# Optimization experiments

Hardware: AMD Instinct MI355X
Metric: run time of the kernel (lower is better)

The kernel has to match this reference:

```python
import jax, jax.numpy as jnp
import numpy as np

B, S, H, E, K, DFF = 4, 2048, 1024, 8, 2, 4096


def setup_inputs() -> dict:
    key = jax.random.key(0)
    k0, k1, k2, k3 = jax.random.split(key, 4)
    sc = 0.02
    return {
        "x": jax.random.normal(k0, (B, S, H), jnp.float32),
        "gate_W": jax.random.normal(k1, (H, E), jnp.float32) * sc,
        "gate_b": jnp.zeros((E,), jnp.float32),
        "W1": jax.random.normal(k2, (H, DFF), jnp.float32) * sc,
        "b1": jnp.zeros((DFF,), jnp.float32),
        "W2": jax.random.normal(k3, (DFF, H), jnp.float32) * sc,
        "b2": jnp.zeros((H,), jnp.float32),
    }


def reference(x, gate_W, gate_b, W1, b1, W2, b2):
    b, s, h = x.shape
    x_flat = x.reshape(-1, h)                      # [T, H]
    gate_scores = x_flat @ gate_W + gate_b         # [T, E]
    top_k_scores, top_k_idx = jax.lax.top_k(gate_scores, K)   # [T, K]
    top_k_w = jax.nn.softmax(top_k_scores, axis=-1)           # [T, K]

    # All experts share the same weights (ModuleList reuses one module), so
    # sum_i w_i * expert_i(x) == expert(x) * sum_i w_i. top_k indices are
    # unique per token, so the per-token combine weight is sum of top-k weights.
    hdd = jax.nn.gelu(x_flat @ W1 + b1, approximate=False)    # [T, DFF]
    y = hdd @ W2 + b2                                         # [T, H]
    tok_w = top_k_w.sum(axis=-1)                              # [T] (== 1.0)
    output = (y * tok_w[:, None]).reshape(b, s, h)

    expert_load = gate_scores.mean(axis=0)                    # [E]
    aux_loss = (expert_load ** 2).sum()
    exp_counts = jnp.zeros((E,), jnp.int32).at[top_k_idx.ravel()].add(1)
    return output, aux_loss, exp_counts
```

## Files before the change

### kernel.cpp

```cpp
#include <hip/hip_runtime.h>
#include <hip/hip_bf16.h>
#include <math.h>

#define Tn   8192
#define Hn   1024
#define En   8
#define DFFn 4096

typedef __attribute__((ext_vector_type(8))) short bf16x8;
typedef __attribute__((ext_vector_type(4))) float f32x4;

static __device__ inline unsigned short f2bf(float f) {
    __hip_bfloat16 h = __float2bfloat16(f);
    return __builtin_bit_cast(unsigned short, h);
}

__global__ __launch_bounds__(256) void prep(
    const float* __restrict__ W1, unsigned short* __restrict__ W1t,
    const float* __restrict__ W2, unsigned short* __restrict__ W2t,
    const float* __restrict__ x, const float* __restrict__ gW,
    const float* __restrict__ gb, unsigned short* __restrict__ xbf,
    float* __restrict__ tokw, float* __restrict__ load_sum,
    int* __restrict__ counts)
{
    __shared__ float smem[8 * 1024 + En];
    __shared__ int   s_cnt[En];
    const int tid = threadIdx.x;
    const int id  = blockIdx.x;

    if (id >= 5120) {
        const int tb = id - 5120;
        float* tile = smem;
        const int bx = tb & 31, by = tb >> 5;
        const int n0 = bx * 32, k0 = by * 32;
        const int r  = tid >> 3, c4 = (tid & 7) * 4;
        float4 v = *(const float4*)(W2 + (size_t)(k0 + r) * Hn + n0 + c4);
        tile[(c4 + 0) * 33 + r] = v.x;
        tile[(c4 + 1) * 33 + r] = v.y;
        tile[(c4 + 2) * 33 + r] = v.z;
        tile[(c4 + 3) * 33 + r] = v.w;
        __syncthreads();
        ushort4 pk;
        pk.x = f2bf(tile[r * 33 + c4 + 0]);
        pk.y = f2bf(tile[r * 33 + c4 + 1]);
        pk.z = f2bf(tile[r * 33 + c4 + 2]);
        pk.w = f2bf(tile[r * 33 + c4 + 3]);
        *(ushort4*)(W2t + (size_t)(n0 + r) * DFFn + k0 + c4) = pk;
        return;
    }

    if (id >= 1024) {
        const int tb = id - 1024;
        float* tile = smem;
        const int bx = tb & 127, by = tb >> 7;
        const int n0 = bx * 32, k0 = by * 32;
        const int r  = tid >> 3, c4 = (tid & 7) * 4;
        float4 v = *(const float4*)(W1 + (size_t)(k0 + r) * DFFn + n0 + c4);
        tile[(c4 + 0) * 33 + r] = v.x;
        tile[(c4 + 1) * 33 + r] = v.y;
        tile[(c4 + 2) * 33 + r] = v.z;
        tile[(c4 + 3) * 33 + r] = v.w;
        __syncthreads();
        ushort4 pk;
        pk.x = f2bf(tile[r * 33 + c4 + 0]);
        pk.y = f2bf(tile[r * 33 + c4 + 1]);
        pk.z = f2bf(tile[r * 33 + c4 + 2]);
        pk.w = f2bf(tile[r * 33 + c4 + 3]);
        *(ushort4*)(W1t + (size_t)(n0 + r) * Hn + k0 + c4) = pk;
        return;
    }

    float* gwt    = smem;
    float* s_load = smem + 8 * 1024;
    if (tid < En) { s_load[tid] = 0.f; s_cnt[tid] = 0; }
    #pragma unroll
    for (int i = 0; i < 32; ++i) {
        int f = tid + i * 256;
        gwt[(f & 7) * 1024 + (f >> 3)] = gW[f];
    }
    __syncthreads();

    const int lane = tid & 63;
    const int wv   = tid >> 6;

    for (int tok = id * 4 + wv; tok < Tn; tok += 4096) {
        const float4* xr = (const float4*)(x + (size_t)tok * Hn);
        float acc[8] = {0.f,0.f,0.f,0.f,0.f,0.f,0.f,0.f};
        #pragma unroll
        for (int j = 0; j < Hn / 256; ++j) {
            int h4 = j * 64 + lane;
            float4 xv = xr[h4];
            ushort4 pk;
            pk.x = f2bf(xv.x); pk.y = f2bf(xv.y);
            pk.z = f2bf(xv.z); pk.w = f2bf(xv.w);
            ((ushort4*)xbf)[(size_t)tok * (Hn / 4) + h4] = pk;
            #pragma unroll
            for (int e = 0; e < 8; ++e) {
                const float4 w = *(const float4*)(gwt + e * 1024 + h4 * 4);
                acc[e] += xv.x * w.x + xv.y * w.y + xv.z * w.z + xv.w * w.w;
            }
        }
        #pragma unroll
        for (int e = 0; e < 8; ++e) {
            float v = acc[e];
            #pragma unroll
            for (int off = 32; off > 0; off >>= 1) v += __shfl_xor(v, off, 64);
            acc[e] = v + gb[e];
        }
        if (lane == 0) {
            #pragma unroll
            for (int e = 0; e < 8; ++e) atomicAdd(&s_load[e], acc[e]);
            int i1 = 0; float v1 = acc[0];
            #pragma unroll
            for (int e = 1; e < 8; ++e) if (acc[e] > v1) { v1 = acc[e]; i1 = e; }
            int i2 = -1; float v2 = -3.0e38f;
            #pragma unroll
            for (int e = 0; e < 8; ++e) if (e != i1 && acc[e] > v2) { v2 = acc[e]; i2 = e; }
            atomicAdd(&s_cnt[i1], 1);
            atomicAdd(&s_cnt[i2], 1);
            float e2 = __expf(v2 - v1);
            float t  = 1.0f + e2;
            tokw[tok] = 1.0f / t + e2 / t;
        }
    }
    __syncthreads();
    if (tid < En) {
        atomicAdd(&load_sum[tid], s_load[tid]);
        atomicAdd(&counts[tid],   s_cnt[tid]);
    }
}


static __device__ inline bf16x8 ldsfrag(const char* base, int row, int chunk) {
    return *(const bf16x8*)(base + row * 128 + (((chunk) ^ (row & 7)) << 4));
}

template<int BN, int WM, int WN, int EPI>
__global__ __launch_bounds__(512, 2) void gemm8(
    const __hip_bfloat16* __restrict__ A,
    const __hip_bfloat16* __restrict__ Bt,
    const float* __restrict__ bias,
    const float* __restrict__ tokw,
    void* __restrict__ C, int N, int K, int nx,
    const float* __restrict__ load_sum, const int* __restrict__ counts,
    float* __restrict__ out_tail, int nblk)
{
    constexpr int BM = 256;
    constexpr int MR = (BM / WM) / 16;
    constexpr int NR = (BN / WN) / 16;
    constexpr int AU = BM / 64;
    constexpr int BU = BN / 64;
    constexpr int ABYTES = BM * 64 * 2;
    constexpr int BBYTES = BN * 64 * 2;
    constexpr int TILEB  = ABYTES + BBYTES;

    extern __shared__ char lds[];

    const int tid = threadIdx.x;
    const int id  = blockIdx.x;

    if (EPI == 0 && id >= nblk) {
        if (tid == 0) {
            float aux = 0.f;
            #pragma unroll
            for (int e = 0; e < En; ++e) {
                float m = load_sum[e] * (1.0f / (float)Tn);
                aux += m * m;
            }
            out_tail[0] = aux;
            #pragma unroll
            for (int e = 0; e < En; ++e) out_tail[1 + e] = (float)counts[e];
        }
        return;
    }

    int wg = id;
    { int xcd = wg & 7, idx = wg >> 3; wg = xcd * (nblk >> 3) + idx; }
    const int by = wg / nx, bx = wg % nx;
    const int m0 = by * BM, n0 = bx * BN;

    const int lane = tid & 63;
    const int wid  = tid >> 6;
    const int wn   = wid % WN;
    const int wm   = wid / WN;
    const int wrow = wm * (BM / WM);
    const int wcol = wn * (BN / WN);
    const int fr   = lane & 15;
    const int fq   = lane >> 4;

    const int sr = tid >> 3;
    const int sc = (tid & 7) ^ (sr & 7);
    unsigned aOff[AU], bOff[BU];
    #pragma unroll
    for (int u = 0; u < AU; ++u)
        aOff[u] = (unsigned)((m0 + u * 64 + sr) * K + sc * 8);
    #pragma unroll
    for (int u = 0; u < BU; ++u)
        bOff[u] = (unsigned)((n0 + u * 64 + sr) * K + sc * 8);

#define STA(b, u, kt) __builtin_amdgcn_global_load_lds( \
    (const __attribute__((address_space(1))) void*)(A + aOff[u] + (unsigned)(kt) * 64u), \
    (__attribute__((address_space(3))) void*)(lds + (b) * TILEB + (u) * 8192 + tid * 16), 16, 0, 0)
#define STB(b, u, kt) __builtin_amdgcn_global_load_lds( \
    (const __attribute__((address_space(1))) void*)(Bt + bOff[u] + (unsigned)(kt) * 64u), \
    (__attribute__((address_space(3))) void*)(lds + (b) * TILEB + ABYTES + (u) * 8192 + tid * 16), 16, 0, 0)

    bf16x8 af[MR / 2][2];
    bf16x8 bfr[4][2];
    f32x4  acc[MR][NR];
    const f32x4 zero = {0.f, 0.f, 0.f, 0.f};
    #pragma unroll
    for (int i = 0; i < MR; ++i)
        #pragma unroll
        for (int j = 0; j < NR; ++j) acc[i][j] = zero;

#define RDA(b, half) do { _Pragma("unroll") \
    for (int m_ = 0; m_ < MR / 2; ++m_) { _Pragma("unroll") \
        for (int ks_ = 0; ks_ < 2; ++ks_) \
            af[m_][ks_] = ldsfrag(lds + (b) * TILEB, \
                wrow + ((half) * (MR / 2) + m_) * 16 + fr, ks_ * 4 + fq); } } while (0)

#define RDB(b, half) do { _Pragma("unroll") \
    for (int n_ = 0; n_ < 2; ++n_) { _Pragma("unroll") \
        for (int ks_ = 0; ks_ < 2; ++ks_) \
            bfr[(half) * 2 + n_][ks_] = ldsfrag(lds + (b) * TILEB + ABYTES, \
                wcol + ((half) * 2 + n_) * 16 + fr, ks_ * 4 + fq); } } while (0)

#define MFMAQ(hm, hn) do { \
    __builtin_amdgcn_s_setprio(1); \
    _Pragma("unroll") \
    for (int m_ = 0; m_ < MR / 2; ++m_) { _Pragma("unroll") \
        for (int n_ = 0; n_ < 2; ++n_) { _Pragma("unroll") \
            for (int ks_ = 0; ks_ < 2; ++ks_) \
                acc[(hm) * (MR / 2) + m_][(hn) * 2 + n_] = \
                    __builtin_amdgcn_mfma_f32_16x16x32_bf16( \
                        bfr[(hn) * 2 + n_][ks_], af[m_][ks_], \
                        acc[(hm) * (MR / 2) + m_][(hn) * 2 + n_], 0, 0, 0); } } \
    __builtin_amdgcn_s_setprio(0); } while (0)

#define MFMAQ1(hm) do { \
    __builtin_amdgcn_s_setprio(1); \
    _Pragma("unroll") \
    for (int m_ = 0; m_ < MR / 2; ++m_) { _Pragma("unroll") \
        for (int n_ = 0; n_ < NR; ++n_) { _Pragma("unroll") \
            for (int ks_ = 0; ks_ < 2; ++ks_) \
                acc[(hm) * (MR / 2) + m_][n_] = \
                    __builtin_amdgcn_mfma_f32_16x16x32_bf16( \
                        bfr[n_][ks_], af[m_][ks_], \
                        acc[(hm) * (MR / 2) + m_][n_], 0, 0, 0); } } \
    __builtin_amdgcn_s_setprio(0); } while (0)

#define MIDSYNC do { \
    __builtin_amdgcn_sched_barrier(0); \
    __builtin_amdgcn_s_barrier(); \
    asm volatile("s_waitcnt lgkmcnt(0)" ::: "memory"); \
    __builtin_amdgcn_sched_barrier(0); } while (0)

#define ENDBAR do { \
    __builtin_amdgcn_sched_barrier(0); \
    __builtin_amdgcn_s_barrier(); \
    __builtin_amdgcn_sched_barrier(0); } while (0)

#define DRAIN6 do { asm volatile("s_waitcnt vmcnt(6)" ::: "memory"); \
    __builtin_amdgcn_sched_barrier(0); } while (0)
#define DRAIN2 do { asm volatile("s_waitcnt vmcnt(2)" ::: "memory"); \
    __builtin_amdgcn_sched_barrier(0); } while (0)

    const int KT = K >> 6;

    if constexpr (WM == 2) {
        STA(0,0,0); STA(0,1,0); STA(0,2,0); STA(0,3,0);
        STB(0,0,0); STB(0,1,0); STB(0,2,0); STB(0,3,0);
        STA(1,0,1); STA(1,2,1);
        STB(1,0,1); STB(1,1,1); STB(1,2,1); STB(1,3,1);
        DRAIN6;
        __builtin_amdgcn_s_barrier();
        __builtin_amdgcn_sched_barrier(0);

        for (int i = 0; i < (KT >> 1); ++i) {
            const int t1 = 2 * i + 1;
            const int c2 = (2 * i + 2 < KT) ? 2 * i + 2 : KT - 1;
            const int c3 = (2 * i + 3 < KT) ? 2 * i + 3 : KT - 1;

            RDA(0, 0); RDB(0, 0);
            STA(1,1,t1); STA(1,3,t1);
            MIDSYNC; MFMAQ(0, 0); ENDBAR;
            RDB(0, 1);
            STA(0,0,c2); STA(0,2,c2);
            MIDSYNC; MFMAQ(0, 1); ENDBAR;
            RDA(0, 1);
            STB(0,0,c2); STB(0,1,c2);
            MIDSYNC; MFMAQ(1, 0); ENDBAR;
            STB(0,2,c2); STB(0,3,c2);
            MIDSYNC; MFMAQ(1, 1); DRAIN6; ENDBAR;
            RDA(1, 0); RDB(1, 0);
            STA(0,1,c2); STA(0,3,c2);
            MIDSYNC; MFMAQ(0, 0); ENDBAR;
            RDB(1, 1);
            STA(1,0,c3); STA(1,2,c3);
            MIDSYNC; MFMAQ(0, 1); ENDBAR;
            RDA(1, 1);
            STB(1,0,c3); STB(1,1,c3);
            MIDSYNC; MFMAQ(1, 0); ENDBAR;
            STB(1,2,c3); STB(1,3,c3);
            MIDSYNC; MFMAQ(1, 1); DRAIN6; ENDBAR;
        }
    } else {
        STA(0,0,0); STA(0,1,0); STA(0,2,0); STA(0,3,0);
        STB(0,0,0); STB(0,1,0);
        STB(1,0,1); STB(1,1,1);
        DRAIN2;
        __builtin_amdgcn_s_barrier();
        __builtin_amdgcn_sched_barrier(0);

        for (int i = 0; i < (KT >> 1); ++i) {
            const int t1 = 2 * i + 1;
            const int c2 = (2 * i + 2 < KT) ? 2 * i + 2 : KT - 1;
            const int c3 = (2 * i + 3 < KT) ? 2 * i + 3 : KT - 1;

            RDA(0, 0); RDB(0, 0); RDB(0, 1);
            STA(1,0,t1); STA(1,1,t1); STA(1,2,t1); STA(1,3,t1);
            MIDSYNC; MFMAQ1(0); ENDBAR;
            RDA(0, 1);
            STB(0,0,c2); STB(0,1,c2);
            MIDSYNC; MFMAQ1(1); DRAIN2; ENDBAR;
            RDA(1, 0); RDB(1, 0); RDB(1, 1);
            STA(0,0,c2); STA(0,1,c2); STA(0,2,c2); STA(0,3,c2);
            MIDSYNC; MFMAQ1(0); ENDBAR;
            RDA(1, 1);
            STB(1,0,c3); STB(1,1,c3);
            MIDSYNC; MFMAQ1(1); DRAIN2; ENDBAR;
        }
    }

    const int mrow0 = m0 + wrow + (lane & 15);
    const int ncol0 = n0 + wcol + (lane >> 4) * 4;
    float4 b4[NR];
    #pragma unroll
    for (int ni = 0; ni < NR; ++ni)
        b4[ni] = *(const float4*)(bias + ncol0 + ni * 16);

    #pragma unroll
    for (int mi = 0; mi < MR; ++mi) {
        const int row = mrow0 + mi * 16;
        float tw = 1.0f;
        if constexpr (EPI == 1) tw = tokw[row];
        #pragma unroll
        for (int ni = 0; ni < NR; ++ni) {
            const int cb = ncol0 + ni * 16;
            f32x4 v = acc[mi][ni];
            v[0] += b4[ni].x; v[1] += b4[ni].y;
            v[2] += b4[ni].z; v[3] += b4[ni].w;
            if constexpr (EPI == 0) {
                ushort4 pk;
                #pragma unroll
                for (int j = 0; j < 4; ++j) {
                    float u  = v[j];
                    float uu = u * u;
                    float z  = u * __fmaf_rn(uu, -0.07135607f, -1.59576912f);
                    float e  = __expf(z);
                    float g  = u * __builtin_amdgcn_rcpf(1.0f + e);
                    ((unsigned short*)&pk)[j] = f2bf(g);
                }
                *(ushort4*)((__hip_bfloat16*)C + (size_t)row * N + cb) = pk;
            } else {
                float4 o;
                o.x = v[0] * tw; o.y = v[1] * tw;
                o.z = v[2] * tw; o.w = v[3] * tw;
                *(float4*)((float*)C + (size_t)row * N + cb) = o;
            }
        }
    }

#undef STA
#undef STB
#undef RDA
#undef RDB
#undef MFMAQ
#undef MFMAQ1
#undef MIDSYNC
#undef ENDBAR
#undef DRAIN6
#undef DRAIN2
}

extern "C" void kernel_launch(void* const* d_in, const int* in_sizes, int n_in,
                              void* d_out, int out_size, void* d_ws, size_t ws_size,
                              hipStream_t stream)
{
    const float* x  = (const float*)d_in[0];
    const float* gW = (const float*)d_in[1];
    const float* gb = (const float*)d_in[2];
    const float* W1 = (const float*)d_in[3];
    const float* b1 = (const float*)d_in[4];
    const float* W2 = (const float*)d_in[5];
    const float* b2 = (const float*)d_in[6];
    float* out = (float*)d_out;

    char* ws = (char*)d_ws;
    __hip_bfloat16* xbf = (__hip_bfloat16*)ws;  ws += (size_t)Tn * Hn * 2;
    __hip_bfloat16* W1t = (__hip_bfloat16*)ws;  ws += (size_t)Hn * DFFn * 2;
    __hip_bfloat16* W2t = (__hip_bfloat16*)ws;  ws += (size_t)Hn * DFFn * 2;
    __hip_bfloat16* hdd = (__hip_bfloat16*)ws;  ws += (size_t)Tn * DFFn * 2;
    float* tokw     = (float*)ws;               ws += (size_t)Tn * 4;
    float* load_sum = (float*)ws;               ws += En * 4;
    int*   counts   = (int*)ws;                 ws += En * 4;

    static bool attr_done = false;
    if (!attr_done) {
        (void)hipFuncSetAttribute(
            reinterpret_cast<const void*>(&gemm8<256, 2, 4, 0>),
            hipFuncAttributeMaxDynamicSharedMemorySize, 131072);
        (void)hipFuncSetAttribute(
            reinterpret_cast<const void*>(&gemm8<128, 4, 2, 1>),
            hipFuncAttributeMaxDynamicSharedMemorySize, 98304);
        attr_done = true;
    }

    hipMemsetAsync(load_sum, 0, En * 4 * 2, stream);

    prep<<<9216, 256, 0, stream>>>(W1, (unsigned short*)W1t,
                                   W2, (unsigned short*)W2t,
                                   x, gW, gb, (unsigned short*)xbf,
                                   tokw, load_sum, counts);

    gemm8<256, 2, 4, 0><<<513, 512, 131072, stream>>>(
        xbf, W1t, b1, nullptr, hdd, DFFn, Hn, 16,
        load_sum, counts, out + (size_t)Tn * Hn, 512);

    gemm8<128, 4, 2, 1><<<256, 512, 98304, stream>>>(
        hdd, W2t, b2, tokw, out, Hn, DFFn, 8,
        nullptr, nullptr, nullptr, 256);
}
```

Baseline: 277.2 us.

## Persist first GEMM over two tiles with overlapped epilogue; larger transpose tiles

The weight-transpose part of prep now uses 128x128 tiles with bf16 conversion before an XOR-swizzled LDS transpose and 16-byte stores. This cuts the block count and LDS traffic. The first GEMM launches half as many blocks, and each block processes two output tiles, issuing the next tile's prologue loads before running the GELU epilogue of the current one. The MFMA operand order is swapped so each lane holds a column layout, and the epilogue uses scalar bf16 stores. These scalar stores may be less efficient, and the hand-tuned vmcnt waits carry a correctness risk.

```diff
diff --git a/kernel.cpp b/kernel.cpp
--- a/kernel.cpp
+++ b/kernel.cpp
@@ -8,6 +8,7 @@
 #define DFFn 4096
 
 typedef __attribute__((ext_vector_type(8))) short bf16x8;
+typedef __attribute__((ext_vector_type(8))) unsigned short u16x8;
 typedef __attribute__((ext_vector_type(4))) float f32x4;
 
 static __device__ inline unsigned short f2bf(float f) {
@@ -28,48 +29,42 @@
     const int tid = threadIdx.x;
     const int id  = blockIdx.x;
 
-    if (id >= 5120) {
-        const int tb = id - 5120;
-        float* tile = smem;
-        const int bx = tb & 31, by = tb >> 5;
-        const int n0 = bx * 32, k0 = by * 32;
-        const int r  = tid >> 3, c4 = (tid & 7) * 4;
-        float4 v = *(const float4*)(W2 + (size_t)(k0 + r) * Hn + n0 + c4);
-        tile[(c4 + 0) * 33 + r] = v.x;
-        tile[(c4 + 1) * 33 + r] = v.y;
-        tile[(c4 + 2) * 33 + r] = v.z;
-        tile[(c4 + 3) * 33 + r] = v.w;
+    if (id < 512) {
+        const float* src; unsigned short* dst; int SR, SC, tb;
+        if (id < 256) { src = W1; dst = W1t; SR = Hn;   SC = DFFn; tb = id; }
+        else          { src = W2; dst = W2t; SR = DFFn; SC = Hn;   tb = id - 256; }
+        const int tcs = SC >> 7;
+        const int tr  = tb / tcs, tc = tb - tr * tcs;
+        const int r0  = tr << 7, c0 = tc << 7;
+        unsigned short* tile = (unsigned short*)smem;
+
+        #pragma unroll
+        for (int i = 0; i < 16; ++i) {
+            int idx = tid + i * 256;
+            int r = idx >> 5, c4 = (idx & 31) << 2;
+            float4 v = *(const float4*)(src + (size_t)(r0 + r) * SC + c0 + c4);
+            int cs = c4 ^ (((r >> 3) & 7) << 2);
+            ushort4 pk;
+            pk.x = f2bf(v.x); pk.y = f2bf(v.y);
+            pk.z = f2bf(v.z); pk.w = f2bf(v.w);
+            *(ushort4*)(tile + r * 128 + cs) = pk;
+        }
         __syncthreads();
-        ushort4 pk;
-        pk.x = f2bf(tile[r * 33 + c4 + 0]);
-        pk.y = f2bf(tile[r * 33 + c4 + 1]);
-        pk.z = f2bf(tile[r * 33 + c4 + 2]);
-        pk.w = f2bf(tile[r * 33 + c4 + 3]);
-        *(ushort4*)(W2t + (size_t)(n0 + r) * DFFn + k0 + c4) = pk;
+        #pragma unroll
+        for (int i = 0; i < 8; ++i) {
+            int idx = tid + i * 256;
+            int n = idx >> 4, kg = idx & 15, k0 = kg << 3;
+            int s = (kg & 7) << 2;
+            u16x8 o;
+            #pragma unroll
+            for (int j = 0; j < 8; ++j)
+                o[j] = tile[(k0 + j) * 128 + (n ^ s)];
+            *(u16x8*)(dst + (size_t)(c0 + n) * SR + r0 + k0) = o;
+        }
         return;
     }
 
-    if (id >= 1024) {
-        const int tb = id - 1024;
-        float* tile = smem;
-        const int bx = tb & 127, by = tb >> 7;
-        const int n0 = bx * 32, k0 = by * 32;
-        const int r  = tid >> 3, c4 = (tid & 7) * 4;
-        float4 v = *(const float4*)(W1 + (size_t)(k0 + r) * DFFn + n0 + c4);
-        tile[(c4 + 0) * 33 + r] = v.x;
-        tile[(c4 + 1) * 33 + r] = v.y;
-        tile[(c4 + 2) * 33 + r] = v.z;
-        tile[(c4 + 3) * 33 + r] = v.w;
-        __syncthreads();
-        ushort4 pk;
-        pk.x = f2bf(tile[r * 33 + c4 + 0]);
-        pk.y = f2bf(tile[r * 33 + c4 + 1]);
-        pk.z = f2bf(tile[r * 33 + c4 + 2]);
-        pk.w = f2bf(tile[r * 33 + c4 + 3]);
-        *(ushort4*)(W1t + (size_t)(n0 + r) * Hn + k0 + c4) = pk;
-        return;
-    }
-
+    const int gid = id - 512;
     float* gwt    = smem;
     float* s_load = smem + 8 * 1024;
     if (tid < En) { s_load[tid] = 0.f; s_cnt[tid] = 0; }
@@ -83,7 +78,7 @@
     const int lane = tid & 63;
     const int wv   = tid >> 6;
 
-    for (int tok = id * 4 + wv; tok < Tn; tok += 4096) {
+    for (int tok = gid * 4 + wv; tok < Tn; tok += 4096) {
         const float4* xr = (const float4*)(x + (size_t)tok * Hn);
         float acc[8] = {0.f,0.f,0.f,0.f,0.f,0.f,0.f,0.f};
         #pragma unroll
@@ -130,12 +125,11 @@
     }
 }
 
-
 static __device__ inline bf16x8 ldsfrag(const char* base, int row, int chunk) {
     return *(const bf16x8*)(base + row * 128 + (((chunk) ^ (row & 7)) << 4));
 }
 
-template<int BN, int WM, int WN, int EPI>
+template<int BN, int WM, int WN, int EPI, int TPB>
 __global__ __launch_bounds__(512, 2) void gemm8(
     const __hip_bfloat16* __restrict__ A,
     const __hip_bfloat16* __restrict__ Bt,
@@ -174,11 +168,6 @@
         return;
     }
 
-    int wg = id;
-    { int xcd = wg & 7, idx = wg >> 3; wg = xcd * (nblk >> 3) + idx; }
-    const int by = wg / nx, bx = wg % nx;
-    const int m0 = by * BM, n0 = bx * BN;
-
     const int lane = tid & 63;
     const int wid  = tid >> 6;
     const int wn   = wid % WN;
@@ -190,13 +179,23 @@
 
     const int sr = tid >> 3;
     const int sc = (tid & 7) ^ (sr & 7);
+
+    int m0, n0;
     unsigned aOff[AU], bOff[BU];
-    #pragma unroll
-    for (int u = 0; u < AU; ++u)
-        aOff[u] = (unsigned)((m0 + u * 64 + sr) * K + sc * 8);
-    #pragma unroll
-    for (int u = 0; u < BU; ++u)
-        bOff[u] = (unsigned)((n0 + u * 64 + sr) * K + sc * 8);
+    auto setup = [&](int t) {
+        int g   = id + t * nblk;
+        int xcd = g & 7;
+        int wg  = xcd * ((nblk * TPB) >> 3) + (g >> 3);
+        int by  = wg / nx, bx = wg - by * nx;
+        m0 = by * BM; n0 = bx * BN;
+        #pragma unroll
+        for (int u = 0; u < AU; ++u)
+            aOff[u] = (unsigned)((m0 + u * 64 + sr) * K + sc * 8);
+        #pragma unroll
+        for (int u = 0; u < BU; ++u)
+            bOff[u] = (unsigned)((n0 + u * 64 + sr) * K + sc * 8);
+    };
+    setup(0);
 
 #define STA(b, u, kt) __builtin_amdgcn_global_load_lds( \
     (const __attribute__((address_space(1))) void*)(A + aOff[u] + (unsigned)(kt) * 64u), \
@@ -204,6 +203,12 @@
 #define STB(b, u, kt) __builtin_amdgcn_global_load_lds( \
     (const __attribute__((address_space(1))) void*)(Bt + bOff[u] + (unsigned)(kt) * 64u), \
     (__attribute__((address_space(3))) void*)(lds + (b) * TILEB + ABYTES + (u) * 8192 + tid * 16), 16, 0, 0)
+
+#define PROLOG_G0 do { \
+    STA(0,0,0); STA(0,1,0); STA(0,2,0); STA(0,3,0); \
+    STB(0,0,0); STB(0,1,0); STB(0,2,0); STB(0,3,0); \
+    STA(1,0,1); STA(1,2,1); \
+    STB(1,0,1); STB(1,1,1); STB(1,2,1); STB(1,3,1); } while (0)
 
     bf16x8 af[MR / 2][2];
     bf16x8 bfr[4][2];
@@ -234,7 +239,7 @@
             for (int ks_ = 0; ks_ < 2; ++ks_) \
                 acc[(hm) * (MR / 2) + m_][(hn) * 2 + n_] = \
                     __builtin_amdgcn_mfma_f32_16x16x32_bf16( \
-                        bfr[(hn) * 2 + n_][ks_], af[m_][ks_], \
+                        af[m_][ks_], bfr[(hn) * 2 + n_][ks_], \
                         acc[(hm) * (MR / 2) + m_][(hn) * 2 + n_], 0, 0, 0); } } \
     __builtin_amdgcn_s_setprio(0); } while (0)
 
@@ -269,41 +274,82 @@
     const int KT = K >> 6;
 
     if constexpr (WM == 2) {
-        STA(0,0,0); STA(0,1,0); STA(0,2,0); STA(0,3,0);
-        STB(0,0,0); STB(0,1,0); STB(0,2,0); STB(0,3,0);
-        STA(1,0,1); STA(1,2,1);
-        STB(1,0,1); STB(1,1,1); STB(1,2,1); STB(1,3,1);
+        PROLOG_G0;
         DRAIN6;
         __builtin_amdgcn_s_barrier();
         __builtin_amdgcn_sched_barrier(0);
 
-        for (int i = 0; i < (KT >> 1); ++i) {
-            const int t1 = 2 * i + 1;
-            const int c2 = (2 * i + 2 < KT) ? 2 * i + 2 : KT - 1;
-            const int c3 = (2 * i + 3 < KT) ? 2 * i + 3 : KT - 1;
-
-            RDA(0, 0); RDB(0, 0);
-            STA(1,1,t1); STA(1,3,t1);
-            MIDSYNC; MFMAQ(0, 0); ENDBAR;
-            RDB(0, 1);
-            STA(0,0,c2); STA(0,2,c2);
-            MIDSYNC; MFMAQ(0, 1); ENDBAR;
-            RDA(0, 1);
-            STB(0,0,c2); STB(0,1,c2);
-            MIDSYNC; MFMAQ(1, 0); ENDBAR;
-            STB(0,2,c2); STB(0,3,c2);
-            MIDSYNC; MFMAQ(1, 1); DRAIN6; ENDBAR;
-            RDA(1, 0); RDB(1, 0);
-            STA(0,1,c2); STA(0,3,c2);
-            MIDSYNC; MFMAQ(0, 0); ENDBAR;
-            RDB(1, 1);
-            STA(1,0,c3); STA(1,2,c3);
-            MIDSYNC; MFMAQ(0, 1); ENDBAR;
-            RDA(1, 1);
-            STB(1,0,c3); STB(1,1,c3);
-            MIDSYNC; MFMAQ(1, 0); ENDBAR;
-            STB(1,2,c3); STB(1,3,c3);
-            MIDSYNC; MFMAQ(1, 1); DRAIN6; ENDBAR;
+        for (int tt = 0; tt < TPB; ++tt) {
+            for (int i = 0; i < (KT >> 1); ++i) {
+                const int t1 = 2 * i + 1;
+                const int c2 = (2 * i + 2 < KT) ? 2 * i + 2 : KT - 1;
+                const int c3 = (2 * i + 3 < KT) ? 2 * i + 3 : KT - 1;
+
+                RDA(0, 0); RDB(0, 0);
+                STA(1,1,t1); STA(1,3,t1);
+                MIDSYNC; MFMAQ(0, 0); ENDBAR;
+                RDB(0, 1);
+                STA(0,0,c2); STA(0,2,c2);
+                MIDSYNC; MFMAQ(0, 1); ENDBAR;
+                RDA(0, 1);
+                STB(0,0,c2); STB(0,1,c2);
+                MIDSYNC; MFMAQ(1, 0); ENDBAR;
+                STB(0,2,c2); STB(0,3,c2);
+                MIDSYNC; MFMAQ(1, 1); DRAIN6; ENDBAR;
+                RDA(1, 0); RDB(1, 0);
+                STA(0,1,c2); STA(0,3,c2);
+                MIDSYNC; MFMAQ(0, 0); ENDBAR;
+                RDB(1, 1);
+                STA(1,0,c3); STA(1,2,c3);
+                MIDSYNC; MFMAQ(0, 1); ENDBAR;
+                RDA(1, 1);
+                STB(1,0,c3); STB(1,1,c3);
+                MIDSYNC; MFMAQ(1, 0); ENDBAR;
+                STB(1,2,c3); STB(1,3,c3);
+                MIDSYNC; MFMAQ(1, 1); DRAIN6; ENDBAR;
+            }
+
+            const int em0 = m0, en0 = n0;
+            if (tt + 1 < TPB) {
+                asm volatile("s_waitcnt vmcnt(0)" ::: "memory");
+                __builtin_amdgcn_sched_barrier(0);
+            }
+            float bias4[NR];
+            #pragma unroll
+            for (int ni = 0; ni < NR; ++ni)
+                bias4[ni] = bias[en0 + wcol + ni * 16 + fr];
+            if (tt + 1 < TPB) {
+                setup(tt + 1);
+                PROLOG_G0;
+            }
+            #pragma unroll
+            for (int mi = 0; mi < MR; ++mi) {
+                #pragma unroll
+                for (int ni = 0; ni < NR; ++ni) {
+                    const int col = en0 + wcol + ni * 16 + fr;
+                    const int rb  = em0 + wrow + mi * 16 + fq * 4;
+                    #pragma unroll
+                    for (int i2 = 0; i2 < 4; ++i2) {
+                        float u  = acc[mi][ni][i2] + bias4[ni];
+                        float uu = u * u;
+                        float z  = u * __fmaf_rn(uu, -0.07135607f, -1.59576912f);
+                        float e  = __expf(z);
+                        float g  = u * __builtin_amdgcn_rcpf(1.0f + e);
+                        ((__hip_bfloat16*)C)[(size_t)(rb + i2) * N + col] =
+                            __float2bfloat16(g);
+                    }
+                }
+            }
+            if (tt + 1 < TPB) {
+                #pragma unroll
+                for (int i = 0; i < MR; ++i)
+                    #pragma unroll
+                    for (int j = 0; j < NR; ++j) acc[i][j] = zero;
+                asm volatile("s_waitcnt vmcnt(38)" ::: "memory");
+                __builtin_amdgcn_sched_barrier(0);
+                __builtin_amdgcn_s_barrier();
+                __builtin_amdgcn_sched_barrier(0);
+            }
         }
     } else {
         STA(0,0,0); STA(0,1,0); STA(0,2,0); STA(0,3,0);
@@ -331,49 +377,34 @@
             STB(1,0,c3); STB(1,1,c3);
             MIDSYNC; MFMAQ1(1); DRAIN2; ENDBAR;
         }
-    }
-
-    const int mrow0 = m0 + wrow + (lane & 15);
-    const int ncol0 = n0 + wcol + (lane >> 4) * 4;
-    float4 b4[NR];
-    #pragma unroll
-    for (int ni = 0; ni < NR; ++ni)
-        b4[ni] = *(const float4*)(bias + ncol0 + ni * 16);
-
-    #pragma unroll
-    for (int mi = 0; mi < MR; ++mi) {
-        const int row = mrow0 + mi * 16;
-        float tw = 1.0f;
-        if constexpr (EPI == 1) tw = tokw[row];
-        #pragma unroll
-        for (int ni = 0; ni < NR; ++ni) {
-            const int cb = ncol0 + ni * 16;
-            f32x4 v = acc[mi][ni];
-            v[0] += b4[ni].x; v[1] += b4[ni].y;
-            v[2] += b4[ni].z; v[3] += b4[ni].w;
-            if constexpr (EPI == 0) {
-                ushort4 pk;
-                #pragma unroll
-                for (int j = 0; j < 4; ++j) {
-                    float u  = v[j];
-                    float uu = u * u;
-                    float z  = u * __fmaf_rn(uu, -0.07135607f, -1.59576912f);
-                    float e  = __expf(z);
-                    float g  = u * __builtin_amdgcn_rcpf(1.0f + e);
-                    ((unsigned short*)&pk)[j] = f2bf(g);
-                }
-                *(ushort4*)((__hip_bfloat16*)C + (size_t)row * N + cb) = pk;
-            } else {
+
+        const int mrow0 = m0 + wrow + fr;
+        const int ncol0 = n0 + wcol + fq * 4;
+        float4 b4[NR];
+        #pragma unroll
+        for (int ni = 0; ni < NR; ++ni)
+            b4[ni] = *(const float4*)(bias + ncol0 + ni * 16);
+
+        #pragma unroll
+        for (int mi = 0; mi < MR; ++mi) {
+            const int row = mrow0 + mi * 16;
+            const float tw = tokw[row];
+            #pragma unroll
+            for (int ni = 0; ni < NR; ++ni) {
+                f32x4 v = acc[mi][ni];
                 float4 o;
-                o.x = v[0] * tw; o.y = v[1] * tw;
-                o.z = v[2] * tw; o.w = v[3] * tw;
-                *(float4*)((float*)C + (size_t)row * N + cb) = o;
+                o.x = (v[0] + b4[ni].x) * tw;
+                o.y = (v[1] + b4[ni].y) * tw;
+                o.z = (v[2] + b4[ni].z) * tw;
+                o.w = (v[3] + b4[ni].w) * tw;
+                *(float4*)((float*)C + (size_t)row * N + ncol0 + ni * 16) = o;
             }
         }
     }
 
 #undef STA
 #undef STB
+#undef PROLOG_G0
 #undef RDA
 #undef RDB
 #undef MFMAQ
@@ -409,26 +440,26 @@
     static bool attr_done = false;
     if (!attr_done) {
         (void)hipFuncSetAttribute(
-            reinterpret_cast<const void*>(&gemm8<256, 2, 4, 0>),
+            reinterpret_cast<const void*>(&gemm8<256, 2, 4, 0, 2>),
             hipFuncAttributeMaxDynamicSharedMemorySize, 131072);
         (void)hipFuncSetAttribute(
-            reinterpret_cast<const void*>(&gemm8<128, 4, 2, 1>),
+            reinterpret_cast<const void*>(&gemm8<128, 4, 2, 1, 1>),
             hipFuncAttributeMaxDynamicSharedMemorySize, 98304);
         attr_done = true;
     }
 
     hipMemsetAsync(load_sum, 0, En * 4 * 2, stream);
 
-    prep<<<9216, 256, 0, stream>>>(W1, (unsigned short*)W1t,
+    prep<<<1536, 256, 0, stream>>>(W1, (unsigned short*)W1t,
                                    W2, (unsigned short*)W2t,
                                    x, gW, gb, (unsigned short*)xbf,
                                    tokw, load_sum, counts);
 
-    gemm8<256, 2, 4, 0><<<513, 512, 131072, stream>>>(
+    gemm8<256, 2, 4, 0, 2><<<257, 512, 131072, stream>>>(
         xbf, W1t, b1, nullptr, hdd, DFFn, Hn, 16,
-        load_sum, counts, out + (size_t)Tn * Hn, 512);
-
-    gemm8<128, 4, 2, 1><<<256, 512, 98304, stream>>>(
+        load_sum, counts, out + (size_t)Tn * Hn, 256);
+
+    gemm8<128, 4, 2, 1, 1><<<256, 512, 98304, stream>>>(
         hdd, W2t, b2, tokw, out, Hn, DFFn, 8,
         nullptr, nullptr, nullptr, 256);
 }
```

Result: slower. 284.7 us (+2.7%).
